# Kernel tuning notes

Hardware: AMD Instinct MI355X
Metric: run time of the kernel (lower is better)

Reference implementation:

```python
import jax, jax.numpy as jnp
import numpy as np

N_FULL = 50000
N_POOL = 12500
E_FULL = 600000
E_POOL = 150000
D = 128


def gcn_conv(x, W, b, edge_index, n):
    """GCNConv with self-loops and symmetric normalization.
    x: [n, d_in], W: [d_in, d_out], edge_index: [2, E] (src -> dst)."""
    xw = x @ W  # [n, d_out]
    loops = jnp.arange(n, dtype=edge_index.dtype)
    src = jnp.concatenate([edge_index[0], loops])
    dst = jnp.concatenate([edge_index[1], loops])
    deg = jnp.zeros((n,), dtype=xw.dtype).at[dst].add(1.0)  # >= 1 (self loops)
    dinv = jax.lax.rsqrt(deg)
    norm = (dinv[src] * dinv[dst])[:, None]  # [E+n, 1]
    out = jax.ops.segment_sum(xw[src] * norm, dst, num_segments=n)
    return out + b


def setup_inputs() -> dict:
    key = jax.random.key(0)
    ks = jax.random.split(key, 8)
    s = 1.0 / np.sqrt(D)
    return {
        "x": jnp.zeros((N_FULL, D), jnp.float32),
        "edge_index": jax.random.randint(ks[0], (2, E_FULL), 0, N_FULL, dtype=jnp.int64)
            if jax.config.jax_enable_x64 else jax.random.randint(ks[0], (2, E_FULL), 0, N_FULL).astype(jnp.int32),
        "pooled_x": jax.random.normal(ks[1], (N_POOL, D), jnp.float32),
        "pooled_edge_index": jax.random.randint(ks[2], (2, E_POOL), 0, N_POOL).astype(jnp.int32),
        "unpool_info": jnp.arange(N_POOL, dtype=jnp.int32),  # unique TopK-kept indices
        "W0": jax.random.normal(ks[3], (D, D), jnp.float32) * s,
        "b0": jnp.zeros((D,), jnp.float32),
        "W1": jax.random.normal(ks[4], (D, D), jnp.float32) * s,
        "b1": jnp.zeros((D,), jnp.float32),
        "W2": jax.random.normal(ks[5], (D, D), jnp.float32) * s,
        "b2": jnp.zeros((D,), jnp.float32),
    }


def reference(x, edge_index, pooled_x, pooled_edge_index, unpool_info,
              W0, b0, W1, b1, W2, b2):
    n = x.shape[0]
    # conv0 on the pooled graph + activation (ELU)
    h = jax.nn.elu(gcn_conv(pooled_x, W0, b0, pooled_edge_index, pooled_x.shape[0]))
    # TopKPool unpool: zero full graph, scatter pooled features to kept indices
    xf = jnp.zeros_like(x).at[unpool_info].set(h)
    # remaining convs on the full graph (dropout=0 / eval mode -> identity)
    xf = jax.nn.elu(gcn_conv(xf, W1, b1, edge_index, n))
    xf = jax.nn.elu(gcn_conv(xf, W2, b2, edge_index, n))
    return xf
```

## Files before the change

### kernel.cpp

```cpp
#include <hip/hip_runtime.h>
#include <math.h>

#define DD 128
#define CF 48
#define C1 16
#define OVF_CAP 4096

static inline int cdiv(long a, long b){ return (int)((a + b - 1) / b); }

typedef __attribute__((ext_vector_type(4))) float f32x4;
typedef __attribute__((ext_vector_type(8))) short bf16x8;
typedef __attribute__((ext_vector_type(4))) short sh4;

__device__ __forceinline__ unsigned short bf16_rn(float f){
  unsigned u = __float_as_uint(f);
  u += 0x7fffu + ((u >> 16) & 1u);
  return (unsigned short)(u >> 16);
}

__global__ void k_init(const int* __restrict__ unpool, int* __restrict__ invm, int npool){
  int i = blockIdx.x * blockDim.x + threadIdx.x;
  if (i < npool) invm[unpool[i]] = i + 1;
}

__global__ void k_build(const int* __restrict__ src_f, const int* __restrict__ dst_f,
                        int nF4, int Ef,
                        int* __restrict__ cnt_f, const int* __restrict__ invm,
                        unsigned* __restrict__ ew2, int4* __restrict__ ovf2, int* __restrict__ novf2,
                        int* __restrict__ rk1, unsigned* __restrict__ ew1,
                        int4* __restrict__ ovf1, int* __restrict__ novf1,
                        const int* __restrict__ src_p, const int* __restrict__ dst_p,
                        int nP4, int Ep,
                        int* __restrict__ cnt_p,
                        unsigned* __restrict__ ew0, int4* __restrict__ ovf0, int* __restrict__ novf0){
  int t = blockIdx.x * blockDim.x + threadIdx.x;
  if (t < nF4){
    int e = t * 4;
    int4 s4 = *(const int4*)(src_f + e);
    int4 d4 = *(const int4*)(dst_f + e);
    int sa[4] = {s4.x, s4.y, s4.z, s4.w};
    int da[4] = {d4.x, d4.y, d4.z, d4.w};
    int ra[4], pa[4];
    #pragma unroll
    for (int i = 0; i < 4; i++) ra[i] = atomicAdd(&cnt_f[da[i]], 1);
    #pragma unroll
    for (int i = 0; i < 4; i++) pa[i] = invm[sa[i]];
    #pragma unroll
    for (int i = 0; i < 4; i++){
      if (ra[i] < CF) ew2[(long)da[i] * CF + ra[i]] = (unsigned)sa[i];
      else { int o = atomicAdd(novf2, 1); if (o < OVF_CAP) ovf2[o] = make_int4(sa[i], 0, da[i], 0); }
    }
    #pragma unroll
    for (int i = 0; i < 4; i++){
      if (pa[i] > 0){
        int pr = pa[i] - 1;
        int r1 = atomicAdd(&rk1[da[i]], 1);
        if (r1 < C1) ew1[(long)da[i] * C1 + r1] = (unsigned)pr;
        else { int o = atomicAdd(novf1, 1); if (o < OVF_CAP) ovf1[o] = make_int4(pr, sa[i], da[i], 0); }
      }
    }
    return;
  }
  t -= nF4;
  int remF = Ef - nF4 * 4;
  if (t < remF){
    int e = nF4 * 4 + t;
    int s = src_f[e], d = dst_f[e];
    int r = atomicAdd(&cnt_f[d], 1);
    if (r < CF) ew2[(long)d * CF + r] = (unsigned)s;
    else { int o = atomicAdd(novf2, 1); if (o < OVF_CAP) ovf2[o] = make_int4(s, 0, d, 0); }
    int pv = invm[s];
    if (pv > 0){
      int pr = pv - 1;
      int r1 = atomicAdd(&rk1[d], 1);
      if (r1 < C1) ew1[(long)d * C1 + r1] = (unsigned)pr;
      else { int o = atomicAdd(novf1, 1); if (o < OVF_CAP) ovf1[o] = make_int4(pr, s, d, 0); }
    }
    return;
  }
  t -= remF;
  if (t < nP4){
    int e = t * 4;
    int4 s4 = *(const int4*)(src_p + e);
    int4 d4 = *(const int4*)(dst_p + e);
    int sa[4] = {s4.x, s4.y, s4.z, s4.w};
    int da[4] = {d4.x, d4.y, d4.z, d4.w};
    int ra[4];
    #pragma unroll
    for (int i = 0; i < 4; i++) ra[i] = atomicAdd(&cnt_p[da[i]], 1);
    #pragma unroll
    for (int i = 0; i < 4; i++){
      if (ra[i] < CF) ew0[(long)da[i] * CF + ra[i]] = (unsigned)sa[i];
      else { int o = atomicAdd(novf0, 1); if (o < OVF_CAP) ovf0[o] = make_int4(sa[i], 0, da[i], 0); }
    }
    return;
  }
  t -= nP4;
  int remP = Ep - nP4 * 4;
  if (t < remP){
    int e = nP4 * 4 + t;
    int s = src_p[e], d = dst_p[e];
    int r = atomicAdd(&cnt_p[d], 1);
    if (r < CF) ew0[(long)d * CF + r] = (unsigned)s;
    else { int o = atomicAdd(novf0, 1); if (o < OVF_CAP) ovf0[o] = make_int4(s, 0, d, 0); }
  }
}

template <int AMODE, bool BF16OUT>
__global__ __launch_bounds__(256, 2) void k_gemm_mfma(const void* __restrict__ Ap,
                                                      const float* __restrict__ W,
                                                      void* __restrict__ Cout, int n){
  __shared__ unsigned short Wl[2][16384];
  const int t    = threadIdx.x;
  const int lane = t & 63;
  const int wv   = t >> 6;
  const int g    = lane >> 4;
  const int r    = lane & 15;

  #pragma unroll
  for (int i = 0; i < 4; i++){
    int item = t + i * 256;
    int kq = item >> 5;
    int c4 = item & 31;
    const float* Wp = W + (long)kq * 512 + c4 * 4;
    float4 ww[4];
    #pragma unroll
    for (int kk = 0; kk < 4; kk++) ww[kk] = *(const float4*)(Wp + kk * 128);
    #pragma unroll
    for (int m = 0; m < 4; m++){
      int c = c4 * 4 + m;
      int boff = c * 256 + (((kq >> 1) ^ (c & 15)) * 16) + (kq & 1) * 8;
      sh4 hq, lq;
      #pragma unroll
      for (int kk = 0; kk < 4; kk++){
        float f = ((const float*)&ww[kk])[m];
        unsigned short hh = bf16_rn(f);
        float hf = __uint_as_float((unsigned)hh << 16);
        hq[kk] = (short)hh;
        lq[kk] = (short)bf16_rn(f - hf);
      }
      *(sh4*)((char*)(&Wl[0][0]) + boff) = hq;
      *(sh4*)((char*)(&Wl[1][0]) + boff) = lq;
    }
  }
  __syncthreads();

  const int rb = blockIdx.x * 128 + wv * 32;
  const int r0 = rb + r, r1 = rb + 16 + r;
  const bool v0 = r0 < n, v1 = r1 < n;

  f32x4 acc[2][8];
  #pragma unroll
  for (int i = 0; i < 2; i++)
    #pragma unroll
    for (int j = 0; j < 8; j++){ f32x4 z = {0.f,0.f,0.f,0.f}; acc[i][j] = z; }

  #pragma unroll
  for (int ks = 0; ks < 4; ks++){
    bf16x8 ah0, al0, ah1, al1;
    if (AMODE == 0){
      const float* pa0 = (const float*)Ap + (long)r0 * DD + g * 8;
      const float* pa1 = (const float*)Ap + (long)r1 * DD + g * 8;
      const float4 z4 = make_float4(0.f,0.f,0.f,0.f);
      float4 a00 = v0 ? *(const float4*)(pa0 + ks * 32)     : z4;
      float4 a01 = v0 ? *(const float4*)(pa0 + ks * 32 + 4) : z4;
      float4 a10 = v1 ? *(const float4*)(pa1 + ks * 32)     : z4;
      float4 a11 = v1 ? *(const float4*)(pa1 + ks * 32 + 4) : z4;
      float f0[8] = {a00.x,a00.y,a00.z,a00.w,a01.x,a01.y,a01.z,a01.w};
      float f1[8] = {a10.x,a10.y,a10.z,a10.w,a11.x,a11.y,a11.z,a11.w};
      #pragma unroll
      for (int i = 0; i < 8; i++){
        unsigned short hh = bf16_rn(f0[i]);
        ah0[i] = (short)hh;
        al0[i] = (short)bf16_rn(f0[i] - __uint_as_float((unsigned)hh << 16));
        unsigned short h1 = bf16_rn(f1[i]);
        ah1[i] = (short)h1;
        al1[i] = (short)bf16_rn(f1[i] - __uint_as_float((unsigned)h1 << 16));
      }
    } else {
      const unsigned* qa0 = (const unsigned*)Ap + (long)r0 * DD + g * 8;
      const unsigned* qa1 = (const unsigned*)Ap + (long)r1 * DD + g * 8;
      const uint4 z4 = make_uint4(0,0,0,0);
      uint4 u00 = v0 ? *(const uint4*)(qa0 + ks * 32)     : z4;
      uint4 u01 = v0 ? *(const uint4*)(qa0 + ks * 32 + 4) : z4;
      uint4 u10 = v1 ? *(const uint4*)(qa1 + ks * 32)     : z4;
      uint4 u11 = v1 ? *(const uint4*)(qa1 + ks * 32 + 4) : z4;
      unsigned uu0[8] = {u00.x,u00.y,u00.z,u00.w,u01.x,u01.y,u01.z,u01.w};
      unsigned uu1[8] = {u10.x,u10.y,u10.z,u10.w,u11.x,u11.y,u11.z,u11.w};
      #pragma unroll
      for (int i = 0; i < 8; i++){
        ah0[i] = (short)(uu0[i] & 0xffffu); al0[i] = (short)(uu0[i] >> 16);
        ah1[i] = (short)(uu1[i] & 0xffffu); al1[i] = (short)(uu1[i] >> 16);
      }
    }
    const int sb = ks * 4 + g;
    #pragma unroll
    for (int cf = 0; cf < 8; cf++){
      const int boff = (cf * 16 + r) * 256 + ((sb ^ r) * 16);
      bf16x8 wh = *(const bf16x8*)((const char*)(&Wl[0][0]) + boff);
      bf16x8 wl = *(const bf16x8*)((const char*)(&Wl[1][0]) + boff);
      acc[0][cf] = __builtin_amdgcn_mfma_f32_16x16x32_bf16(ah0, wh, acc[0][cf], 0, 0, 0);
      acc[1][cf] = __builtin_amdgcn_mfma_f32_16x16x32_bf16(ah1, wh, acc[1][cf], 0, 0, 0);
      acc[0][cf] = __builtin_amdgcn_mfma_f32_16x16x32_bf16(al0, wh, acc[0][cf], 0, 0, 0);
      acc[1][cf] = __builtin_amdgcn_mfma_f32_16x16x32_bf16(al1, wh, acc[1][cf], 0, 0, 0);
      acc[0][cf] = __builtin_amdgcn_mfma_f32_16x16x32_bf16(ah0, wl, acc[0][cf], 0, 0, 0);
      acc[1][cf] = __builtin_amdgcn_mfma_f32_16x16x32_bf16(ah1, wl, acc[1][cf], 0, 0, 0);
    }
  }

  #pragma unroll
  for (int rf = 0; rf < 2; rf++){
    #pragma unroll
    for (int cf = 0; cf < 8; cf++){
      #pragma unroll
      for (int e = 0; e < 4; e++){
        int row = rb + rf * 16 + g * 4 + e;
        if (row < n){
          float v = acc[rf][cf][e];
          if (BF16OUT)
            ((unsigned short*)Cout)[(long)row * DD + cf * 16 + r] = bf16_rn(v);
          else
            ((float*)Cout)[(long)row * DD + cf * 16 + r] = v;
        }
      }
    }
  }
}

__global__ __launch_bounds__(256) void k_agg0(const float* __restrict__ xw,
    const int* __restrict__ cnt, const unsigned* __restrict__ ew,
    const int4* __restrict__ ovf, const int* __restrict__ novf,
    const float* __restrict__ b, unsigned* __restrict__ outp, int n){
  int row = __builtin_amdgcn_readfirstlane(blockIdx.x * 4 + (threadIdx.x >> 6));
  if (row >= n) return;
  int c = (threadIdx.x & 63) * 2;
  int deg = __builtin_amdgcn_readfirstlane(cnt[row]);
  int m = deg < CF ? deg : CF;
  long base = (long)row * CF;
  float ax[8], ay[8];
  #pragma unroll
  for (int i = 0; i < 8; i++){ ax[i] = 0.f; ay[i] = 0.f; }
  for (int j0 = 0; j0 < m; j0 += 16){
    uint4 q0 = *(const uint4*)(ew + base + j0);
    uint4 q1 = *(const uint4*)(ew + base + j0 + 4);
    uint4 q2 = *(const uint4*)(ew + base + j0 + 8);
    uint4 q3 = *(const uint4*)(ew + base + j0 + 12);
    unsigned ua[16] = {q0.x,q0.y,q0.z,q0.w, q1.x,q1.y,q1.z,q1.w,
                       q2.x,q2.y,q2.z,q2.w, q3.x,q3.y,q3.z,q3.w};
    float2 v[16]; float w[16];
    #pragma unroll
    for (int i = 0; i < 16; i++){
      bool val = (j0 + i) < m;
      int s = val ? (int)ua[i] : row;
      w[i] = val ? rsqrtf((float)cnt[s] + 1.f) : 0.f;
      v[i] = *(const float2*)(xw + (long)s * DD + c);
    }
    #pragma unroll
    for (int i = 0; i < 16; i++){
      ax[i & 7] += v[i].x * w[i];
      ay[i & 7] += v[i].y * w[i];
    }
  }
  int no = __builtin_amdgcn_readfirstlane(novf[0]);
  if (no > 0){
    no = no < OVF_CAP ? no : OVF_CAP;
    for (int k = 0; k < no; k++){
      int4 od = ovf[k];
      if (od.z == row){
        float w = rsqrtf((float)cnt[od.x] + 1.f);
        float2 v = *(const float2*)(xw + (long)od.x * DD + c);
        ax[0] += v.x * w; ay[0] += v.y * w;
      }
    }
  }
  float sax = ((ax[0]+ax[1])+(ax[2]+ax[3])) + ((ax[4]+ax[5])+(ax[6]+ax[7]));
  float say = ((ay[0]+ay[1])+(ay[2]+ay[3])) + ((ay[4]+ay[5])+(ay[6]+ay[7]));
  float dd = rsqrtf((float)deg + 1.f);
  float2 sv = *(const float2*)(xw + (long)row * DD + c);
  float2 bb = *(const float2*)(b + c);
  float vx = sax * dd + sv.x * dd * dd + bb.x;
  float vy = say * dd + sv.y * dd * dd + bb.y;
  vx = vx > 0.f ? vx : expm1f(vx);
  vy = vy > 0.f ? vy : expm1f(vy);
  unsigned short hx = bf16_rn(vx);
  unsigned short lx = bf16_rn(vx - __uint_as_float((unsigned)hx << 16));
  unsigned short hy = bf16_rn(vy);
  unsigned short ly = bf16_rn(vy - __uint_as_float((unsigned)hy << 16));
  *(uint2*)(outp + (long)row * DD + c) =
      make_uint2((unsigned)hx | ((unsigned)lx << 16), (unsigned)hy | ((unsigned)ly << 16));
}

__global__ __launch_bounds__(256) void k_agg1(const unsigned short* __restrict__ hwb,
    const int* __restrict__ invm, const int* __restrict__ cnt_f,
    const int* __restrict__ rk1, const unsigned* __restrict__ ew,
    const int* __restrict__ unpool,
    const int4* __restrict__ ovf, const int* __restrict__ novf,
    const float* __restrict__ b, unsigned* __restrict__ outp, int n){
  int row = __builtin_amdgcn_readfirstlane(blockIdx.x * 4 + (threadIdx.x >> 6));
  if (row >= n) return;
  int c = (threadIdx.x & 63) * 2;
  int m1 = __builtin_amdgcn_readfirstlane(rk1[row]);
  if (m1 > C1) m1 = C1;
  int deg = __builtin_amdgcn_readfirstlane(cnt_f[row]);
  long base = (long)row * C1;
  int pv = __builtin_amdgcn_readfirstlane(invm[row]);
  float ax[8], ay[8];
  #pragma unroll
  for (int i = 0; i < 8; i++){ ax[i] = 0.f; ay[i] = 0.f; }
  if (m1 > 0){
    uint4 q0 = *(const uint4*)(ew + base);
    uint4 q1 = *(const uint4*)(ew + base + 4);
    uint4 q2 = *(const uint4*)(ew + base + 8);
    uint4 q3 = *(const uint4*)(ew + base + 12);
    unsigned ua[16] = {q0.x,q0.y,q0.z,q0.w, q1.x,q1.y,q1.z,q1.w,
                       q2.x,q2.y,q2.z,q2.w, q3.x,q3.y,q3.z,q3.w};
    unsigned v[16]; float w[16];
    #pragma unroll
    for (int i = 0; i < 16; i++){
      bool val = i < m1;
      int pr = val ? (int)ua[i] : 0;
      int s  = val ? unpool[pr] : 0;
      w[i] = val ? rsqrtf((float)cnt_f[s] + 1.f) : 0.f;
      v[i] = *(const unsigned*)(hwb + (long)pr * DD + c);
    }
    #pragma unroll
    for (int i = 0; i < 16; i++){
      ax[i & 7] += __uint_as_float(v[i] << 16) * w[i];
      ay[i & 7] += __uint_as_float(v[i] & 0xffff0000u) * w[i];
    }
  }
  int no = __builtin_amdgcn_readfirstlane(novf[0]);
  if (no > 0){
    no = no < OVF_CAP ? no : OVF_CAP;
    for (int k = 0; k < no; k++){
      int4 od = ovf[k];
      if (od.z == row){
        float w = rsqrtf((float)cnt_f[od.y] + 1.f);
        unsigned v = *(const unsigned*)(hwb + (long)od.x * DD + c);
        ax[0] += __uint_as_float(v << 16) * w;
        ay[0] += __uint_as_float(v & 0xffff0000u) * w;
      }
    }
  }
  float sax = ((ax[0]+ax[1])+(ax[2]+ax[3])) + ((ax[4]+ax[5])+(ax[6]+ax[7]));
  float say = ((ay[0]+ay[1])+(ay[2]+ay[3])) + ((ay[4]+ay[5])+(ay[6]+ay[7]));
  float dd = rsqrtf((float)deg + 1.f);
  float sx = 0.f, sy = 0.f;
  if (pv > 0){
    unsigned sv = *(const unsigned*)(hwb + (long)(pv - 1) * DD + c);
    sx = __uint_as_float(sv << 16); sy = __uint_as_float(sv & 0xffff0000u);
  }
  float2 bb = *(const float2*)(b + c);
  float vx = sax * dd + sx * dd * dd + bb.x;
  float vy = say * dd + sy * dd * dd + bb.y;
  vx = vx > 0.f ? vx : expm1f(vx);
  vy = vy > 0.f ? vy : expm1f(vy);
  unsigned short hx = bf16_rn(vx);
  unsigned short lx = bf16_rn(vx - __uint_as_float((unsigned)hx << 16));
  unsigned short hy = bf16_rn(vy);
  unsigned short ly = bf16_rn(vy - __uint_as_float((unsigned)hy << 16));
  *(uint2*)(outp + (long)row * DD + c) =
      make_uint2((unsigned)hx | ((unsigned)lx << 16), (unsigned)hy | ((unsigned)ly << 16));
}

__global__ __launch_bounds__(256) void k_agg2(const unsigned short* __restrict__ xwb,
    const int* __restrict__ cnt, const unsigned* __restrict__ ew,
    const int4* __restrict__ ovf, const int* __restrict__ novf,
    const float* __restrict__ b, float* __restrict__ out, int n){
  int row = __builtin_amdgcn_readfirstlane(blockIdx.x * 4 + (threadIdx.x >> 6));
  if (row >= n) return;
  int c = (threadIdx.x & 63) * 2;
  int deg = __builtin_amdgcn_readfirstlane(cnt[row]);
  int m = deg < CF ? deg : CF;
  long base = (long)row * CF;
  float ax[8], ay[8];
  #pragma unroll
  for (int i = 0; i < 8; i++){ ax[i] = 0.f; ay[i] = 0.f; }
  for (int j0 = 0; j0 < m; j0 += 16){
    uint4 q0 = *(const uint4*)(ew + base + j0);
    uint4 q1 = *(const uint4*)(ew + base + j0 + 4);
    uint4 q2 = *(const uint4*)(ew + base + j0 + 8);
    uint4 q3 = *(const uint4*)(ew + base + j0 + 12);
    unsigned ua[16] = {q0.x,q0.y,q0.z,q0.w, q1.x,q1.y,q1.z,q1.w,
                       q2.x,q2.y,q2.z,q2.w, q3.x,q3.y,q3.z,q3.w};
    unsigned v[16]; float w[16];
    #pragma unroll
    for (int i = 0; i < 16; i++){
      bool val = (j0 + i) < m;
      int s = val ? (int)ua[i] : row;
      w[i] = val ? rsqrtf((float)cnt[s] + 1.f) : 0.f;
      v[i] = *(const unsigned*)(xwb + (long)s * DD + c);
    }
    #pragma unroll
    for (int i = 0; i < 16; i++){
      ax[i & 7] += __uint_as_float(v[i] << 16) * w[i];
      ay[i & 7] += __uint_as_float(v[i] & 0xffff0000u) * w[i];
    }
  }
  int no = __builtin_amdgcn_readfirstlane(novf[0]);
  if (no > 0){
    no = no < OVF_CAP ? no : OVF_CAP;
    for (int k = 0; k < no; k++){
      int4 od = ovf[k];
      if (od.z == row){
        float w = rsqrtf((float)cnt[od.x] + 1.f);
        unsigned v = *(const unsigned*)(xwb + (long)od.x * DD + c);
        ax[0] += __uint_as_float(v << 16) * w;
        ay[0] += __uint_as_float(v & 0xffff0000u) * w;
      }
    }
  }
  float sax = ((ax[0]+ax[1])+(ax[2]+ax[3])) + ((ax[4]+ax[5])+(ax[6]+ax[7]));
  float say = ((ay[0]+ay[1])+(ay[2]+ay[3])) + ((ay[4]+ay[5])+(ay[6]+ay[7]));
  float dd = rsqrtf((float)deg + 1.f);
  unsigned sv = *(const unsigned*)(xwb + (long)row * DD + c);
  float sx = __uint_as_float(sv << 16), sy = __uint_as_float(sv & 0xffff0000u);
  float2 bb = *(const float2*)(b + c);
  float vx = sax * dd + sx * dd * dd + bb.x;
  float vy = say * dd + sy * dd * dd + bb.y;
  vx = vx > 0.f ? vx : expm1f(vx);
  vy = vy > 0.f ? vy : expm1f(vy);
  *(float2*)(out + (long)row * DD + c) = make_float2(vx, vy);
}

extern "C" void kernel_launch(void* const* d_in, const int* in_sizes, int n_in,
                              void* d_out, int out_size, void* d_ws, size_t ws_size,
                              hipStream_t stream) {
  const int*   edge   = (const int*)d_in[1];
  const float* px     = (const float*)d_in[2];
  const int*   pedge  = (const int*)d_in[3];
  const int*   unpool = (const int*)d_in[4];
  const float* W0 = (const float*)d_in[5]; const float* b0 = (const float*)d_in[6];
  const float* W1 = (const float*)d_in[7]; const float* b1 = (const float*)d_in[8];
  const float* W2 = (const float*)d_in[9]; const float* b2 = (const float*)d_in[10];
  const int n_full = in_sizes[0] / DD;
  const int E_full = in_sizes[1] / 2;
  const int n_pool = in_sizes[2] / DD;
  const int E_pool = in_sizes[3] / 2;
  float* out = (float*)d_out;

  char* w = (char*)d_ws;
  size_t off = 0;
  auto alloc = [&](size_t bytes) -> void* {
    void* p = (void*)(w + off);
    off += (bytes + 255) / 256 * 256;
    return p;
  };
  int* cnt_f = (int*)alloc((size_t)n_full * 4);
  int* cnt_p = (int*)alloc((size_t)n_pool * 4);
  int* rk1   = (int*)alloc((size_t)n_full * 4);
  int* novf3 = (int*)alloc(12);
  int* invm  = (int*)alloc((size_t)n_full * 4);
  size_t zspan = (size_t)((char*)(invm + n_full) - (char*)cnt_f);
  unsigned* ew2 = (unsigned*)alloc((size_t)n_full * CF * 4);
  unsigned* ew1 = (unsigned*)alloc((size_t)n_full * C1 * 4);
  unsigned* ew0 = (unsigned*)alloc((size_t)n_pool * CF * 4);
  int4* ovf2 = (int4*)alloc((size_t)OVF_CAP * 16);
  int4* ovf1 = (int4*)alloc((size_t)OVF_CAP * 16);
  int4* ovf0 = (int4*)alloc((size_t)OVF_CAP * 16);
  const size_t big = (size_t)n_full * DD * 4;
  float* bufA = (float*)alloc(big);
  float* bufB = (float*)alloc(big);

  const int* src_f = edge;          const int* dst_f = edge + E_full;
  const int* src_p = pedge;         const int* dst_p = pedge + E_pool;

  const int nF4 = E_full / 4, remF = E_full & 3;
  const int nP4 = E_pool / 4, remP = E_pool & 3;

  (void)hipMemsetAsync(cnt_f, 0, zspan, stream);
  k_init<<<cdiv(n_pool, 256), 256, 0, stream>>>(unpool, invm, n_pool);
  k_build<<<cdiv((long)nF4 + remF + nP4 + remP, 256), 256, 0, stream>>>(
      src_f, dst_f, nF4, E_full, cnt_f, invm,
      ew2, ovf2, novf3 + 0,
      rk1, ew1, ovf1, novf3 + 1,
      src_p, dst_p, nP4, E_pool, cnt_p,
      ew0, ovf0, novf3 + 2);

  float* xw0            = bufA;
  unsigned* h0p         = (unsigned*)bufB;
  unsigned short* hw1b  = (unsigned short*)bufA;
  unsigned* y1p         = (unsigned*)bufB;
  unsigned short* xw2b  = (unsigned short*)bufA;

  k_gemm_mfma<0,false><<<cdiv(n_pool,128),256,0,stream>>>(px, W0, xw0, n_pool);
  k_agg0<<<cdiv(n_pool,4),256,0,stream>>>(xw0, cnt_p, ew0, ovf0, novf3 + 2, b0, h0p, n_pool);

  k_gemm_mfma<1,true><<<cdiv(n_pool,128),256,0,stream>>>(h0p, W1, hw1b, n_pool);
  k_agg1<<<cdiv(n_full,4),256,0,stream>>>(hw1b, invm, cnt_f, rk1, ew1, unpool,
                                          ovf1, novf3 + 1, b1, y1p, n_full);

  k_gemm_mfma<1,true><<<cdiv(n_full,128),256,0,stream>>>(y1p, W2, xw2b, n_full);
  k_agg2<<<cdiv(n_full,4),256,0,stream>>>(xw2b, cnt_f, ew2, ovf2, novf3 + 0, b2, out, n_full);
}
```

Measured before the change: 275.3 us.

## Split edge build into count-rank pass and fill pass, fold invm init

The edge-bucket build becomes two passes. The first computes each edge's per-destination rank with atomics and writes it to a rank array; it also fills the unpool inverse map, replacing the separate init kernel. The second pass reads the ranks and scatters the source indices into the bucket arrays. The aim is to separate the atomic latency from the dependent scattered writes and to drop one launch, at the cost of an extra kernel and extra rank-array traffic.

```diff
diff --git a/kernel.cpp b/kernel.cpp
--- a/kernel.cpp
+++ b/kernel.cpp
@@ -18,31 +18,63 @@
   return (unsigned short)(u >> 16);
 }
 
-__global__ void k_init(const int* __restrict__ unpool, int* __restrict__ invm, int npool){
-  int i = blockIdx.x * blockDim.x + threadIdx.x;
-  if (i < npool) invm[unpool[i]] = i + 1;
-}
-
-__global__ void k_build(const int* __restrict__ src_f, const int* __restrict__ dst_f,
-                        int nF4, int Ef,
-                        int* __restrict__ cnt_f, const int* __restrict__ invm,
-                        unsigned* __restrict__ ew2, int4* __restrict__ ovf2, int* __restrict__ novf2,
-                        int* __restrict__ rk1, unsigned* __restrict__ ew1,
-                        int4* __restrict__ ovf1, int* __restrict__ novf1,
-                        const int* __restrict__ src_p, const int* __restrict__ dst_p,
-                        int nP4, int Ep,
-                        int* __restrict__ cnt_p,
-                        unsigned* __restrict__ ew0, int4* __restrict__ ovf0, int* __restrict__ novf0){
+__global__ void k_count(const int* __restrict__ dst_f, int nF4, int Ef,
+                        int* __restrict__ cnt_f, int* __restrict__ rank_f,
+                        const int* __restrict__ dst_p, int nP4, int Ep,
+                        int* __restrict__ cnt_p, int* __restrict__ rank_p,
+                        const int* __restrict__ unpool, int* __restrict__ invm, int npool){
+  int t = blockIdx.x * blockDim.x + threadIdx.x;
+  if (t < nF4){
+    int e = t * 4;
+    int4 d = *(const int4*)(dst_f + e);
+    int r0 = atomicAdd(&cnt_f[d.x], 1);
+    int r1 = atomicAdd(&cnt_f[d.y], 1);
+    int r2 = atomicAdd(&cnt_f[d.z], 1);
+    int r3 = atomicAdd(&cnt_f[d.w], 1);
+    *(int4*)(rank_f + e) = make_int4(r0, r1, r2, r3);
+    return;
+  }
+  t -= nF4;
+  int remF = Ef - nF4 * 4;
+  if (t < remF){ int e = nF4 * 4 + t; rank_f[e] = atomicAdd(&cnt_f[dst_f[e]], 1); return; }
+  t -= remF;
+  if (t < nP4){
+    int e = t * 4;
+    int4 d = *(const int4*)(dst_p + e);
+    int r0 = atomicAdd(&cnt_p[d.x], 1);
+    int r1 = atomicAdd(&cnt_p[d.y], 1);
+    int r2 = atomicAdd(&cnt_p[d.z], 1);
+    int r3 = atomicAdd(&cnt_p[d.w], 1);
+    *(int4*)(rank_p + e) = make_int4(r0, r1, r2, r3);
+    return;
+  }
+  t -= nP4;
+  int remP = Ep - nP4 * 4;
+  if (t < remP){ int e = nP4 * 4 + t; rank_p[e] = atomicAdd(&cnt_p[dst_p[e]], 1); return; }
+  t -= remP;
+  if (t < npool) invm[unpool[t]] = t + 1;
+}
+
+__global__ void k_fill(const int* __restrict__ src_f, const int* __restrict__ dst_f,
+                       int nF4, int Ef,
+                       const int* __restrict__ rank_f, const int* __restrict__ invm,
+                       unsigned* __restrict__ ew2, int4* __restrict__ ovf2, int* __restrict__ novf2,
+                       int* __restrict__ rk1, unsigned* __restrict__ ew1,
+                       int4* __restrict__ ovf1, int* __restrict__ novf1,
+                       const int* __restrict__ src_p, const int* __restrict__ dst_p,
+                       int nP4, int Ep,
+                       const int* __restrict__ rank_p,
+                       unsigned* __restrict__ ew0, int4* __restrict__ ovf0, int* __restrict__ novf0){
   int t = blockIdx.x * blockDim.x + threadIdx.x;
   if (t < nF4){
     int e = t * 4;
     int4 s4 = *(const int4*)(src_f + e);
     int4 d4 = *(const int4*)(dst_f + e);
+    int4 r4 = *(const int4*)(rank_f + e);
     int sa[4] = {s4.x, s4.y, s4.z, s4.w};
     int da[4] = {d4.x, d4.y, d4.z, d4.w};
-    int ra[4], pa[4];
-    #pragma unroll
-    for (int i = 0; i < 4; i++) ra[i] = atomicAdd(&cnt_f[da[i]], 1);
+    int ra[4] = {r4.x, r4.y, r4.z, r4.w};
+    int pa[4];
     #pragma unroll
     for (int i = 0; i < 4; i++) pa[i] = invm[sa[i]];
     #pragma unroll
@@ -65,8 +97,7 @@
   int remF = Ef - nF4 * 4;
   if (t < remF){
     int e = nF4 * 4 + t;
-    int s = src_f[e], d = dst_f[e];
-    int r = atomicAdd(&cnt_f[d], 1);
+    int s = src_f[e], d = dst_f[e], r = rank_f[e];
     if (r < CF) ew2[(long)d * CF + r] = (unsigned)s;
     else { int o = atomicAdd(novf2, 1); if (o < OVF_CAP) ovf2[o] = make_int4(s, 0, d, 0); }
     int pv = invm[s];
@@ -83,11 +114,10 @@
     int e = t * 4;
     int4 s4 = *(const int4*)(src_p + e);
     int4 d4 = *(const int4*)(dst_p + e);
+    int4 r4 = *(const int4*)(rank_p + e);
     int sa[4] = {s4.x, s4.y, s4.z, s4.w};
     int da[4] = {d4.x, d4.y, d4.z, d4.w};
-    int ra[4];
-    #pragma unroll
-    for (int i = 0; i < 4; i++) ra[i] = atomicAdd(&cnt_p[da[i]], 1);
+    int ra[4] = {r4.x, r4.y, r4.z, r4.w};
     #pragma unroll
     for (int i = 0; i < 4; i++){
       if (ra[i] < CF) ew0[(long)da[i] * CF + ra[i]] = (unsigned)sa[i];
@@ -99,8 +129,7 @@
   int remP = Ep - nP4 * 4;
   if (t < remP){
     int e = nP4 * 4 + t;
-    int s = src_p[e], d = dst_p[e];
-    int r = atomicAdd(&cnt_p[d], 1);
+    int s = src_p[e], d = dst_p[e], r = rank_p[e];
     if (r < CF) ew0[(long)d * CF + r] = (unsigned)s;
     else { int o = atomicAdd(novf0, 1); if (o < OVF_CAP) ovf0[o] = make_int4(s, 0, d, 0); }
   }
@@ -452,6 +481,8 @@
   int* novf3 = (int*)alloc(12);
   int* invm  = (int*)alloc((size_t)n_full * 4);
   size_t zspan = (size_t)((char*)(invm + n_full) - (char*)cnt_f);
+  int* rank_f = (int*)alloc((size_t)E_full * 4);
+  int* rank_p = (int*)alloc((size_t)E_pool * 4);
   unsigned* ew2 = (unsigned*)alloc((size_t)n_full * CF * 4);
   unsigned* ew1 = (unsigned*)alloc((size_t)n_full * C1 * 4);
   unsigned* ew0 = (unsigned*)alloc((size_t)n_pool * CF * 4);
@@ -469,12 +500,15 @@
   const int nP4 = E_pool / 4, remP = E_pool & 3;
 
   (void)hipMemsetAsync(cnt_f, 0, zspan, stream);
-  k_init<<<cdiv(n_pool, 256), 256, 0, stream>>>(unpool, invm, n_pool);
-  k_build<<<cdiv((long)nF4 + remF + nP4 + remP, 256), 256, 0, stream>>>(
-      src_f, dst_f, nF4, E_full, cnt_f, invm,
+  k_count<<<cdiv((long)nF4 + remF + nP4 + remP + n_pool, 256), 256, 0, stream>>>(
+      dst_f, nF4, E_full, cnt_f, rank_f,
+      dst_p, nP4, E_pool, cnt_p, rank_p,
+      unpool, invm, n_pool);
+  k_fill<<<cdiv((long)nF4 + remF + nP4 + remP, 256), 256, 0, stream>>>(
+      src_f, dst_f, nF4, E_full, rank_f, invm,
       ew2, ovf2, novf3 + 0,
       rk1, ew1, ovf1, novf3 + 1,
-      src_p, dst_p, nP4, E_pool, cnt_p,
+      src_p, dst_p, nP4, E_pool, rank_p,
       ew0, ovf0, novf3 + 2);
 
   float* xw0            = bufA;
```

Result: no change. 277.8 us (+0.9%).
